# Kernel optimization log

Hardware: AMD Instinct MI355X
Metric: run time of the kernel (lower is better)

## Reference

```python
import jax, jax.numpy as jnp
import numpy as np

D_MODEL = 512
N_HEAD = 8
D_HEAD = 64
N_LAYER = 4
D_INNER = 2048
IN_CH = 2048
N_CLS = 64
B, T = 2, 2048
LN_EPS = 1e-5


def layer_norm(x, s, b):
    mu = jnp.mean(x, axis=-1, keepdims=True)
    var = jnp.mean(jnp.square(x - mu), axis=-1, keepdims=True)
    return (x - mu) * jax.lax.rsqrt(var + LN_EPS) * s + b


def rel_shift(x):
    # x: [q, k, b, n] -> Transformer-XL relative shift
    q, k, b, n = x.shape
    zp = jnp.zeros((q, 1, b, n), x.dtype)
    x = jnp.concatenate([zp, x], axis=1)          # [q, k+1, b, n]
    x = x.reshape(k + 1, q, b, n)[1:]             # drop first row
    return x.reshape(q, k, b, n)


def setup_inputs() -> dict:
    key = jax.random.key(0)
    ks = jax.random.split(key, 12)
    s = 0.02
    return {
        "x": jax.random.normal(ks[0], (B, IN_CH, T), jnp.float32),
        "emb_w": jax.random.normal(ks[1], (D_MODEL, IN_CH), jnp.float32) * s,
        "emb_b": jnp.zeros((D_MODEL,), jnp.float32),
        "r_w_bias": jax.random.normal(ks[2], (N_HEAD, D_HEAD), jnp.float32) * s,
        "r_r_bias": jax.random.normal(ks[3], (N_HEAD, D_HEAD), jnp.float32) * s,
        "qkv_w": jax.random.normal(ks[4], (N_LAYER, 3 * N_HEAD * D_HEAD, D_MODEL), jnp.float32) * s,
        "qkv_b": jnp.zeros((N_LAYER, 3 * N_HEAD * D_HEAD), jnp.float32),
        "r_proj_w": jax.random.normal(ks[5], (N_LAYER, N_HEAD * D_HEAD, D_MODEL), jnp.float32) * s,
        "o_w": jax.random.normal(ks[6], (N_LAYER, D_MODEL, N_HEAD * D_HEAD), jnp.float32) * s,
        "ln1_s": jnp.ones((N_LAYER, D_MODEL), jnp.float32),
        "ln1_b": jnp.zeros((N_LAYER, D_MODEL), jnp.float32),
        "ff1_w": jax.random.normal(ks[7], (N_LAYER, D_INNER, D_MODEL), jnp.float32) * s,
        "ff1_b": jnp.zeros((N_LAYER, D_INNER), jnp.float32),
        "ff2_w": jax.random.normal(ks[8], (N_LAYER, D_MODEL, D_INNER), jnp.float32) * s,
        "ff2_b": jnp.zeros((N_LAYER, D_MODEL), jnp.float32),
        "ln2_s": jnp.ones((N_LAYER, D_MODEL), jnp.float32),
        "ln2_b": jnp.zeros((N_LAYER, D_MODEL), jnp.float32),
        "cls_w": jax.random.normal(ks[9], (N_CLS, D_MODEL), jnp.float32) * s,
        "cls_b": jnp.zeros((N_CLS,), jnp.float32),
    }


def reference(x, emb_w, emb_b, r_w_bias, r_r_bias, qkv_w, qkv_b, r_proj_w, o_w,
              ln1_s, ln1_b, ff1_w, ff1_b, ff2_w, ff2_b, ln2_s, ln2_b, cls_w, cls_b):
    b, _, t = x.shape
    d = D_MODEL
    # 1x1 conv embedding, then to [T, B, d_model] layout as in _forward
    h = jnp.einsum('dc,bct->tbd', emb_w, x) + emb_b

    # sinusoidal positional embedding over pos_seq = klen-1 .. 0 (klen == qlen, mem_len=0)
    pos_seq = jnp.arange(t - 1, -1, -1, dtype=h.dtype)
    inv_freq = 1.0 / (10000.0 ** (jnp.arange(0, d, 2, dtype=h.dtype) / d))
    sinusoid = pos_seq[:, None] * inv_freq[None, :]
    pos_emb = jnp.concatenate([jnp.sin(sinusoid), jnp.cos(sinusoid)], axis=-1)  # [T, d]

    scale = 1.0 / (D_HEAD ** 0.5)
    for i in range(N_LAYER):
        w = h
        heads = jnp.einsum('ed,tbd->tbe', qkv_w[i], w) + qkv_b[i]          # [T,B,3*H*Dh]
        q, k, v = jnp.split(heads, 3, axis=-1)
        q = q.reshape(t, b, N_HEAD, D_HEAD)
        k = k.reshape(t, b, N_HEAD, D_HEAD)
        v = v.reshape(t, b, N_HEAD, D_HEAD)
        r_head_k = jnp.einsum('ed,td->te', r_proj_w[i], pos_emb).reshape(t, N_HEAD, D_HEAD)

        AC = jnp.einsum('ibnd,jbnd->ijbn', q + r_w_bias, k)                # content term
        BD = rel_shift(jnp.einsum('ibnd,jnd->ijbn', q + r_r_bias, r_head_k))  # position term
        attn_prob = jax.nn.softmax((AC + BD) * scale, axis=1)              # softmax over keys
        attn_vec = jnp.einsum('ijbn,jbnd->ibnd', attn_prob, v).reshape(t, b, N_HEAD * D_HEAD)
        attn_out = jnp.einsum('de,tbe->tbd', o_w[i], attn_vec)             # o_net (no bias)
        h = layer_norm(w + attn_out, ln1_s[i], ln1_b[i])                   # post-lnorm

        ff = jnp.einsum('fd,tbd->tbf', ff1_w[i], h) + ff1_b[i]
        ff = jax.nn.relu(ff)
        ff = jnp.einsum('df,tbf->tbd', ff2_w[i], ff) + ff2_b[i]
        h = layer_norm(h + ff, ln2_s[i], ln2_b[i])

    # 1x1 conv classifier -> [B, num_classes, T]
    out = jnp.einsum('kd,tbd->bkt', cls_w, h) + cls_b[None, :, None]
    return out
```

## Files before the change

kernel.cpp:

```cpp
#include <hip/hip_runtime.h>
#include <hip/hip_bf16.h>
#include <math.h>


#define T_   2048
#define B_   2
#define DM   512
#define NH   8
#define DH   64
#define DI   2048
#define INCH 2048
#define NCLS 64
#define MT   4096

typedef __attribute__((ext_vector_type(8))) short short8;
typedef __attribute__((ext_vector_type(4))) float float4v;

#define QSCALE 0.1803368801111204f

__device__ inline ushort f2bf(float f) {
  uint u = __float_as_uint(f);
  return (ushort)((u + 0x7FFFu + ((u >> 16) & 1u)) >> 16);
}
__device__ inline float bf2f(ushort h) { return __uint_as_float(((uint)h) << 16); }
__device__ inline uint pkbf(float a, float b) {
  __hip_bfloat162 h = __float22bfloat162_rn(float2{a, b});
  return *(uint*)&h;
}
__device__ inline void gload16(const void* g, void* lds) {
  __builtin_amdgcn_global_load_lds(
      (const __attribute__((address_space(1))) void*)g,
      (__attribute__((address_space(3))) void*)lds, 16, 0, 0);
}

__global__ __launch_bounds__(256) void pos_kernel(ushort* __restrict__ pe) {
  int idx = blockIdx.x * 256 + threadIdx.x;
  if (idx >= T_ * DM) return;
  int t = idx >> 9;
  int i = idx & 511;
  int j = (i < 256) ? i : (i - 256);
  double invf = exp(-(double)(2 * j) * (9.210340371976184 / 512.0));
  double a = (double)(T_ - 1 - t) * invf;
  pe[idx] = f2bf((i < 256) ? (float)sin(a) : (float)cos(a));
}

__global__ __launch_bounds__(256) void cvt6_kernel(
    const float* s0, ushort* d0, int n0,
    const float* s1, ushort* d1, int n1,
    const float* s2, ushort* d2, int n2,
    const float* s3, ushort* d3, int n3,
    const float* s4, ushort* d4, int n4,
    const float* s5, ushort* d5, int n5)
{
  const float* s; ushort* d; int n;
  switch (blockIdx.y) {
    case 0: s = s0; d = d0; n = n0; break;
    case 1: s = s1; d = d1; n = n1; break;
    case 2: s = s2; d = d2; n = n2; break;
    case 3: s = s3; d = d3; n = n3; break;
    case 4: s = s4; d = d4; n = n4; break;
    default: s = s5; d = d5; n = n5; break;
  }
  int i = blockIdx.x * 256 + threadIdx.x;
  if (i >= n) return;
  float4 v = ((const float4*)s)[i];
  ushort4 w = { f2bf(v.x), f2bf(v.y), f2bf(v.z), f2bf(v.w) };
  ((ushort4*)d)[i] = w;
}

__global__ __launch_bounds__(256) void xpose_kernel(const float* __restrict__ x,
                                                    ushort* __restrict__ xb) {
  __shared__ float s[32][33];
  int t0 = blockIdx.x * 32, k0 = blockIdx.y * 32, b = blockIdx.z;
  int tx = threadIdx.x & 31, ty = threadIdx.x >> 5;
#pragma unroll
  for (int l = 0; l < 4; ++l) {
    int k = k0 + ty + l * 8;
    s[ty + l * 8][tx] = x[((size_t)b * INCH + k) * T_ + t0 + tx];
  }
  __syncthreads();
#pragma unroll
  for (int l = 0; l < 4; ++l) {
    int t = t0 + ty + l * 8;
    xb[((size_t)(t * 2 + b)) * INCH + k0 + tx] = f2bf(s[tx][ty + l * 8]);
  }
}

__global__ __launch_bounds__(256) void vtrans_kernel(const ushort* __restrict__ heads,
                                                     ushort* __restrict__ vtg) {
  __shared__ ushort s[64][72];
  const int tid = threadIdx.x;
  int t0 = blockIdx.x * 64;
  int b = blockIdx.y & 1, n = blockIdx.y >> 1;
  for (int e = tid; e < 512; e += 256) {
    int r = e >> 3, c = e & 7;
    *(uint4*)&s[r][c * 8] =
        *(const uint4*)&heads[(size_t)((t0 + r) * 2 + b) * 1536 + 1024 + n * 64 + c * 8];
  }
  __syncthreads();
  for (int e = tid; e < 512; e += 256) {
    int d = e >> 3, c = e & 7;
    ushort tmp[8];
#pragma unroll
    for (int j = 0; j < 8; ++j) tmp[j] = s[c * 8 + j][d];
    *(uint4*)&vtg[((size_t)((b * 8 + n) * 64 + d)) * (size_t)T_ + t0 + c * 8] = *(uint4*)tmp;
  }
}

template<int TM, int OUTMODE, bool RELU>
__global__ __launch_bounds__(256) void gemm_bf16(
    const ushort* __restrict__ A, const ushort* __restrict__ W,
    const float* __restrict__ bias, float* __restrict__ Cf, ushort* __restrict__ Cb,
    int M, int N, int K)
{
  __shared__ __attribute__((aligned(16))) ushort As[TM * 64];
  __shared__ __attribute__((aligned(16))) ushort Bs[128 * 64];
  const int NI = TM / 32;
  const int tid  = threadIdx.x;
  const int wave = tid >> 6, lane = tid & 63;
  const int quad = lane >> 4, lidx = lane & 15;
  const int m0 = blockIdx.y * TM, n0 = blockIdx.x * 128;
  const int r8 = lane >> 3;
  const int cs = ((lane & 7) ^ (r8 & 7)) * 8;

  float4v acc[NI * 4];
#pragma unroll
  for (int i = 0; i < NI * 4; ++i) acc[i] = (float4v){0.f, 0.f, 0.f, 0.f};

  const int wm = (wave >> 1) * (TM / 2), wn = (wave & 1) * 64;

  for (int k0 = 0; k0 < K; k0 += 64) {
    __syncthreads();
#pragma unroll
    for (int g = 0; g < TM / 32; ++g) {
      int r0 = wave * 8 + g * 32;
      gload16(A + (size_t)(m0 + r0 + r8) * K + k0 + cs, &As[r0 * 64]);
    }
#pragma unroll
    for (int g = 0; g < 4; ++g) {
      int r0 = wave * 8 + g * 32;
      gload16(W + (size_t)(n0 + r0 + r8) * K + k0 + cs, &Bs[r0 * 64]);
    }
    __syncthreads();

#pragma unroll
    for (int kb = 0; kb < 2; ++kb) {
      short8 af[NI], bf4[4];
      const int ch = (((kb * 4 + quad) ^ (lidx & 7)) * 8);
#pragma unroll
      for (int i = 0; i < NI; ++i)
        af[i] = *(const short8*)&As[(wm + i * 16 + lidx) * 64 + ch];
#pragma unroll
      for (int j = 0; j < 4; ++j)
        bf4[j] = *(const short8*)&Bs[(wn + j * 16 + lidx) * 64 + ch];
#pragma unroll
      for (int i = 0; i < NI; ++i)
#pragma unroll
        for (int j = 0; j < 4; ++j)
          acc[i * 4 + j] = __builtin_amdgcn_mfma_f32_16x16x32_bf16(af[i], bf4[j], acc[i * 4 + j], 0, 0, 0);
    }
  }

  float bj[4];
#pragma unroll
  for (int j = 0; j < 4; ++j) bj[j] = bias ? bias[n0 + wn + j * 16 + lidx] : 0.f;
#pragma unroll
  for (int i = 0; i < NI; ++i) {
    int rbase = m0 + wm + i * 16 + quad * 4;
#pragma unroll
    for (int j = 0; j < 4; ++j) {
      int col = n0 + wn + j * 16 + lidx;
#pragma unroll
      for (int reg = 0; reg < 4; ++reg) {
        float v = acc[i * 4 + j][reg] + bj[j];
        if (RELU) v = fmaxf(v, 0.f);
        size_t off = (size_t)(rbase + reg) * N + col;
        if (OUTMODE != 1) Cf[off] = v;
        if (OUTMODE != 0) Cb[off] = f2bf(v);
      }
    }
  }
}

#define BM 128
#define BN 128
#define BK 16
#define LDT 132

__global__ __launch_bounds__(256) void gemm_f32(
    const float* __restrict__ A, const float* __restrict__ W,
    const float* __restrict__ bias, float* __restrict__ C,
    int M, int N, int K)
{
  __shared__ float Asm[BK][LDT];
  __shared__ float Wsm[BK][LDT];
  const int tid = threadIdx.x;
  const int m0 = blockIdx.y * BM;
  const int n0 = blockIdx.x * BN;
  const int row = tid >> 1;
  const int kh  = (tid & 1) * 8;
  const int ty  = tid >> 4;
  const int tx  = tid & 15;

  float acc[8][8];
#pragma unroll
  for (int i = 0; i < 8; ++i)
#pragma unroll
    for (int j = 0; j < 8; ++j) acc[i][j] = 0.f;

  for (int kt = 0; kt < K; kt += BK) {
    float a_reg[8], w_reg[8];
    {
      const float* ap = A + (size_t)(m0 + row) * K + (kt + kh);
      float4 v0 = *(const float4*)ap;
      float4 v1 = *(const float4*)(ap + 4);
      a_reg[0] = v0.x; a_reg[1] = v0.y; a_reg[2] = v0.z; a_reg[3] = v0.w;
      a_reg[4] = v1.x; a_reg[5] = v1.y; a_reg[6] = v1.z; a_reg[7] = v1.w;
    }
    {
      int nn = n0 + row;
      if (nn < N) {
        const float* wp = W + (size_t)nn * K + (kt + kh);
        float4 v0 = *(const float4*)wp;
        float4 v1 = *(const float4*)(wp + 4);
        w_reg[0] = v0.x; w_reg[1] = v0.y; w_reg[2] = v0.z; w_reg[3] = v0.w;
        w_reg[4] = v1.x; w_reg[5] = v1.y; w_reg[6] = v1.z; w_reg[7] = v1.w;
      } else {
#pragma unroll
        for (int q = 0; q < 8; ++q) w_reg[q] = 0.f;
      }
    }
    __syncthreads();
#pragma unroll
    for (int q = 0; q < 8; ++q) { Asm[kh + q][row] = a_reg[q]; Wsm[kh + q][row] = w_reg[q]; }
    __syncthreads();
#pragma unroll
    for (int k = 0; k < BK; ++k) {
      float4 a0 = *(const float4*)&Asm[k][ty * 4];
      float4 a1 = *(const float4*)&Asm[k][ty * 4 + 64];
      float4 b0 = *(const float4*)&Wsm[k][tx * 4];
      float4 b1 = *(const float4*)&Wsm[k][tx * 4 + 64];
      float av[8] = {a0.x, a0.y, a0.z, a0.w, a1.x, a1.y, a1.z, a1.w};
      float bv[8] = {b0.x, b0.y, b0.z, b0.w, b1.x, b1.y, b1.z, b1.w};
#pragma unroll
      for (int i = 0; i < 8; ++i)
#pragma unroll
        for (int j = 0; j < 8; ++j) acc[i][j] += av[i] * bv[j];
    }
  }

#pragma unroll
  for (int ih = 0; ih < 2; ++ih)
#pragma unroll
    for (int i = 0; i < 4; ++i) {
      int m = m0 + ty * 4 + ih * 64 + i;
#pragma unroll
      for (int jh = 0; jh < 2; ++jh) {
        int nn = n0 + tx * 4 + jh * 64;
        if (nn < N) {
          float4 v;
          v.x = acc[ih * 4 + i][jh * 4 + 0] + bias[nn + 0];
          v.y = acc[ih * 4 + i][jh * 4 + 1] + bias[nn + 1];
          v.z = acc[ih * 4 + i][jh * 4 + 2] + bias[nn + 2];
          v.w = acc[ih * 4 + i][jh * 4 + 3] + bias[nn + 3];
          *(float4*)&C[(size_t)m * N + nn] = v;
        }
      }
    }
}

#define GT 68

__device__ inline short8 bfrag(const char* base, int lidx, int quad, int kb) {
  return *(const short8*)(base + lidx * 128 + ((((kb << 2) + quad) ^ (lidx & 7)) << 4));
}

__global__ __launch_bounds__(256, 2) void attn_mfma_kernel(
    const ushort* __restrict__ heads, const ushort* __restrict__ rk,
    const ushort* __restrict__ vtg,
    const float* __restrict__ rwb, const float* __restrict__ rrb,
    ushort* __restrict__ avec)
{
  __shared__ __attribute__((aligned(16))) ushort Ks[64 * 64];
  __shared__ __attribute__((aligned(16))) ushort Vt[64 * 64];
  __shared__ __attribute__((aligned(16))) ushort Re[128 * 64];
  __shared__ __attribute__((aligned(16))) ushort Gbt[128 * GT];
  __shared__ __attribute__((aligned(16))) ushort Pb[64 * 64];

  const int tid  = threadIdx.x;
  const int i0   = blockIdx.x * 64;
  const int b    = blockIdx.y & 1;
  const int n    = blockIdx.y >> 1;
  const int wave = tid >> 6;
  const int lane = tid & 63;
  const int quad = lane >> 4;
  const int lidx = lane & 15;
  const int r8   = lane >> 3;
  const int cs8  = ((lane & 7) ^ (r8 & 7)) * 8;
  const int bn64 = (b * 8 + n) * 64;

  short8 qw[4][2], qr[4][2], q4[2];
  {
    auto qfrag = [&](int row, int kb, const float* bias) -> short8 {
      short8 q;
      if (row < T_) q = *(const short8*)&heads[(size_t)(row * 2 + b) * 1536 + n * 64 + kb * 32 + quad * 8];
      else { for (int t = 0; t < 8; ++t) ((ushort*)&q)[t] = 0; }
      short8 o;
#pragma unroll
      for (int t = 0; t < 8; ++t) {
        float f = (bf2f((ushort)((ushort*)&q)[t]) + bias[n * 64 + kb * 32 + quad * 8 + t]) * QSCALE;
        ((ushort*)&o)[t] = f2bf(f);
      }
      return o;
    };
#pragma unroll
    for (int rt = 0; rt < 4; ++rt) {
      int row = i0 + rt * 16 + lidx;
      qw[rt][0] = qfrag(row, 0, rwb); qw[rt][1] = qfrag(row, 1, rwb);
      qr[rt][0] = qfrag(row, 0, rrb); qr[rt][1] = qfrag(row, 1, rrb);
    }
    int row4 = i0 + 64 + lidx;
    q4[0] = qfrag(row4, 0, rrb); q4[1] = qfrag(row4, 1, rrb);
  }

  const int cfix = wave * 16 + lidx;

  int addrG0[16], addrP[16];
#pragma unroll
  for (int rt = 0; rt < 4; ++rt)
#pragma unroll
    for (int reg = 0; reg < 4; ++reg) {
      int rloc = rt * 16 + quad * 4 + reg;
      addrG0[rt * 4 + reg] = (cfix + 63 - rloc) * GT + rloc;
      addrP[rt * 4 + reg]  = rloc * 64 + (((cfix >> 3) ^ (rloc & 7)) * 8) + (cfix & 7);
    }

  float4v oacc[4], liacc[4];
#pragma unroll
  for (int rt = 0; rt < 4; ++rt) {
    oacc[rt]  = (float4v){0.f, 0.f, 0.f, 0.f};
    liacc[rt] = (float4v){0.f, 0.f, 0.f, 0.f};
  }
  short8 ones8;
#pragma unroll
  for (int t = 0; t < 8; ++t) ((ushort*)&ones8)[t] = 0x3F80;

  auto stageKRe = [&](int jt) {
    int j0 = jt * 64, qmin = j0 + 1984 - i0;
#pragma unroll
    for (int half = 0; half < 2; ++half) {
      int r0 = 8 * wave + 32 * half;
      gload16(heads + (size_t)((j0 + r0 + r8) * 2 + b) * 1536 + 512 + n * 64 + cs8, &Ks[r0 * 64]);
    }
#pragma unroll
    for (int q4i = 0; q4i < 4; ++q4i) {
      int r0 = 8 * wave + 32 * q4i;
      int qh = qmin + r0 + r8;
      int p  = (qh > T_) ? (qh - T_ - 1) : ((qh == T_) ? 0 : qh);
      gload16(rk + (size_t)p * 2048 + n * 64 + cs8, &Re[r0 * 64]);
    }
  };
  auto stageV = [&](int jt) {
    int j0 = jt * 64;
#pragma unroll
    for (int half = 0; half < 2; ++half) {
      int r0 = 8 * wave + 32 * half;
      gload16(vtg + (size_t)(bn64 + r0 + r8) * (size_t)T_ + j0 + cs8, &Vt[r0 * 64]);
    }
  };
  auto fixup = [&](int jt) {
    int qmin = jt * 64 + 1984 - i0;
    int Tidx = T_ - qmin;
    if (Tidx >= 0 && Tidx < 128) {
      if (tid < 32) ((uint*)Re)[Tidx * 32 + tid] = 0u;
      __syncthreads();
    }
  };

  stageKRe(0);
  stageV(0);
  __syncthreads();
  fixup(0);

  for (int jt = 0; jt < 32; ++jt) {
    const int qmin = jt * 64 + 1984 - i0;
    const int wth  = T_ - qmin;

    float4v sv[4];
    {
      const char* KsW = (const char*)Ks + wave * 2048;
      short8 k0 = bfrag(KsW, lidx, quad, 0);
      short8 k1 = bfrag(KsW, lidx, quad, 1);
#pragma unroll
      for (int rt = 0; rt < 4; ++rt) {
        float4v c = {0.f, 0.f, 0.f, 0.f};
        c = __builtin_amdgcn_mfma_f32_16x16x32_bf16(qw[rt][0], k0, c, 0, 0, 0);
        c = __builtin_amdgcn_mfma_f32_16x16x32_bf16(qw[rt][1], k1, c, 0, 0, 0);
        sv[rt] = c;
      }
    }
#pragma unroll
    for (int si = 0; si < 2; ++si) {
      const int ws = wave + si * 4;
      const int w0 = ws * 16;
      const char* ReW = (const char*)Re + w0 * 128;
      short8 rb0 = bfrag(ReW, lidx, quad, 0);
      short8 rb1 = bfrag(ReW, lidx, quad, 1);
#pragma unroll
      for (int rt = 0; rt < 4; ++rt) {
        bool need = si == 0 ? (rt >= 3 - wave) : (rt <= 3 - wave);
        if (need) {
          float4v g = {0.f, 0.f, 0.f, 0.f};
          g = __builtin_amdgcn_mfma_f32_16x16x32_bf16(qr[rt][0], rb0, g, 0, 0, 0);
          g = __builtin_amdgcn_mfma_f32_16x16x32_bf16(qr[rt][1], rb1, g, 0, 0, 0);
          uint2 st; st.x = pkbf(g[0], g[1]); st.y = pkbf(g[2], g[3]);
          *(uint2*)&Gbt[(w0 + lidx) * GT + rt * 16 + quad * 4] = st;
        }
      }
      if (si == 0 && wth < 63) {
        float4v g = {0.f, 0.f, 0.f, 0.f};
        g = __builtin_amdgcn_mfma_f32_16x16x32_bf16(q4[0], rb0, g, 0, 0, 0);
        g = __builtin_amdgcn_mfma_f32_16x16x32_bf16(q4[1], rb1, g, 0, 0, 0);
        if (quad == 0) Gbt[(w0 + lidx) * GT + 64] = f2bf(g[0]);
      }
    }
    __syncthreads();

    {
      const int selb = cfix + 63 - wth;
#pragma unroll
      for (int rt = 0; rt < 4; ++rt)
#pragma unroll
        for (int reg = 0; reg < 4; ++reg) {
          const int idx = rt * 4 + reg;
          const int rloc = rt * 16 + quad * 4 + reg;
          int ga = addrG0[idx] + ((rloc < selb) ? 1 : 0);
          float x = sv[rt][reg] + bf2f(Gbt[ga]);
          Pb[addrP[idx]] = f2bf(exp2f(x));
        }
    }
    __syncthreads();

    if (jt < 31) stageKRe(jt + 1);

    {
      const char* VtW = (const char*)Vt + wave * 2048;
      short8 vb0 = bfrag(VtW, lidx, quad, 0);
      short8 vb1 = bfrag(VtW, lidx, quad, 1);
#pragma unroll
      for (int rt = 0; rt < 4; ++rt) {
        const char* PbW = (const char*)Pb + rt * 2048;
        short8 pa0 = bfrag(PbW, lidx, quad, 0);
        short8 pa1 = bfrag(PbW, lidx, quad, 1);
        oacc[rt]  = __builtin_amdgcn_mfma_f32_16x16x32_bf16(pa0, vb0, oacc[rt], 0, 0, 0);
        oacc[rt]  = __builtin_amdgcn_mfma_f32_16x16x32_bf16(pa1, vb1, oacc[rt], 0, 0, 0);
        liacc[rt] = __builtin_amdgcn_mfma_f32_16x16x32_bf16(pa0, ones8, liacc[rt], 0, 0, 0);
        liacc[rt] = __builtin_amdgcn_mfma_f32_16x16x32_bf16(pa1, ones8, liacc[rt], 0, 0, 0);
      }
    }
    __syncthreads();

    if (jt < 31) {
      stageV(jt + 1);
      fixup(jt + 1);
    }
  }

#pragma unroll
  for (int rt = 0; rt < 4; ++rt)
#pragma unroll
    for (int reg = 0; reg < 4; ++reg) {
      int i = i0 + rt * 16 + quad * 4 + reg;
      float val = oacc[rt][reg] / liacc[rt][reg];
      avec[(size_t)(i * 2 + b) * DM + n * 64 + wave * 16 + lidx] = f2bf(val);
    }
}

__global__ __launch_bounds__(256) void ln_res_kernel(
    float* __restrict__ h, ushort* __restrict__ hb, const float* __restrict__ delta,
    const float* __restrict__ s, const float* __restrict__ bb)
{
  const int m = blockIdx.x;
  const int tid = threadIdx.x;
  float* hp = h + (size_t)m * DM;
  ushort* hbp = hb + (size_t)m * DM;
  const float* dp = delta + (size_t)m * DM;
  float x0 = hp[tid] + dp[tid];
  float x1 = hp[tid + 256] + dp[tid + 256];
  float sum = x0 + x1, sq = x0 * x0 + x1 * x1;
#pragma unroll
  for (int o = 32; o > 0; o >>= 1) { sum += __shfl_down(sum, o); sq += __shfl_down(sq, o); }
  __shared__ float part[8];
  int wv = tid >> 6;
  if ((tid & 63) == 0) { part[wv * 2] = sum; part[wv * 2 + 1] = sq; }
  __syncthreads();
  float ts = part[0] + part[2] + part[4] + part[6];
  float tq = part[1] + part[3] + part[5] + part[7];
  float mu = ts * (1.f / DM);
  float var = tq * (1.f / DM) - mu * mu;
  float rs = rsqrtf(var + 1e-5f);
  float y0 = (x0 - mu) * rs * s[tid]       + bb[tid];
  float y1 = (x1 - mu) * rs * s[tid + 256] + bb[tid + 256];
  hp[tid] = y0;       hbp[tid] = f2bf(y0);
  hp[tid + 256] = y1; hbp[tid + 256] = f2bf(y1);
}

__global__ __launch_bounds__(256) void reorder_kernel(const float* __restrict__ ct,
                                                      float* __restrict__ out) {
  int idx = blockIdx.x * 256 + threadIdx.x;
  if (idx >= B_ * NCLS * T_) return;
  int t  = idx & (T_ - 1);
  int nc = (idx >> 11) & 63;
  int bb = idx >> 17;
  out[idx] = ct[(size_t)(t * B_ + bb) * NCLS + nc];
}

extern "C" void kernel_launch(void* const* d_in, const int* in_sizes, int n_in,
                              void* d_out, int out_size, void* d_ws, size_t ws_size,
                              hipStream_t stream)
{
  const float* x     = (const float*)d_in[0];
  const float* emb_w = (const float*)d_in[1];
  const float* emb_b = (const float*)d_in[2];
  const float* rwb   = (const float*)d_in[3];
  const float* rrb   = (const float*)d_in[4];
  const float* qkv_w = (const float*)d_in[5];
  const float* qkv_b = (const float*)d_in[6];
  const float* rproj = (const float*)d_in[7];
  const float* o_w   = (const float*)d_in[8];
  const float* ln1s  = (const float*)d_in[9];
  const float* ln1b  = (const float*)d_in[10];
  const float* ff1w  = (const float*)d_in[11];
  const float* ff1b  = (const float*)d_in[12];
  const float* ff2w  = (const float*)d_in[13];
  const float* ff2b  = (const float*)d_in[14];
  const float* ln2s  = (const float*)d_in[15];
  const float* ln2b  = (const float*)d_in[16];
  const float* clsw  = (const float*)d_in[17];
  const float* clsb  = (const float*)d_in[18];
  float* out = (float*)d_out;

  char* p = (char*)d_ws;
  float*  h       = (float*)p;   p += (size_t)MT * DM * 4;
  float*  tmpf    = (float*)p;   p += (size_t)MT * DM * 4;
  ushort* hb      = (ushort*)p;  p += (size_t)MT * DM * 2;
  ushort* headsb  = (ushort*)p;  p += (size_t)MT * 1536 * 2;
  ushort* peb     = (ushort*)p;  p += (size_t)T_ * DM * 2;
  ushort* rk_all  = (ushort*)p;  p += (size_t)T_ * 2048 * 2;
  ushort* avecb   = (ushort*)p;  p += (size_t)MT * DM * 2;
  ushort* xfb     = (ushort*)p;  p += (size_t)MT * INCH * 2;
  ushort* emb_wb  = (ushort*)p;  p += (size_t)DM * INCH * 2;
  ushort* qkv_wb  = (ushort*)p;  p += (size_t)4 * 1536 * DM * 2;
  ushort* rproj_wb= (ushort*)p;  p += (size_t)4 * DM * DM * 2;
  ushort* o_wb    = (ushort*)p;  p += (size_t)4 * DM * DM * 2;
  ushort* ff1_wb  = (ushort*)p;  p += (size_t)4 * DI * DM * 2;
  ushort* ff2_wb  = (ushort*)p;  p += (size_t)4 * DM * DI * 2;
  ushort* vtg     = xfb;

  cvt6_kernel<<<dim3(4096, 6), 256, 0, stream>>>(
      emb_w, emb_wb, DM * INCH / 4,
      qkv_w, qkv_wb, 4 * 1536 * DM / 4,
      rproj, rproj_wb, 4 * DM * DM / 4,
      o_w,   o_wb,   4 * DM * DM / 4,
      ff1w,  ff1_wb, 4 * DI * DM / 4,
      ff2w,  ff2_wb, 4 * DM * DI / 4);
  pos_kernel<<<(T_ * DM) / 256, 256, 0, stream>>>(peb);
  xpose_kernel<<<dim3(T_ / 32, INCH / 32, B_), 256, 0, stream>>>(x, xfb);

  gemm_bf16<64, 2, false><<<dim3(DM / 128, MT / 64), 256, 0, stream>>>(
      xfb, emb_wb, emb_b, h, hb, MT, DM, INCH);
  gemm_bf16<128, 1, false><<<dim3(2048 / 128, T_ / 128), 256, 0, stream>>>(
      peb, rproj_wb, nullptr, nullptr, rk_all, T_, 2048, DM);

  for (int l = 0; l < 4; ++l) {
    gemm_bf16<128, 1, false><<<dim3(1536 / 128, MT / 128), 256, 0, stream>>>(
        hb, qkv_wb + (size_t)l * 1536 * DM, qkv_b + l * 1536, nullptr, headsb, MT, 1536, DM);
    vtrans_kernel<<<dim3(T_ / 64, B_ * NH), 256, 0, stream>>>(headsb, vtg);
    attn_mfma_kernel<<<dim3(T_ / 64, B_ * NH), 256, 0, stream>>>(
        headsb, rk_all + (size_t)l * 512, vtg, rwb, rrb, avecb);
    gemm_bf16<32, 0, false><<<dim3(DM / 128, MT / 32), 256, 0, stream>>>(
        avecb, o_wb + (size_t)l * DM * DM, nullptr, tmpf, nullptr, MT, DM, DM);
    ln_res_kernel<<<MT, 256, 0, stream>>>(h, hb, tmpf, ln1s + l * DM, ln1b + l * DM);
    gemm_bf16<128, 1, true><<<dim3(DI / 128, MT / 128), 256, 0, stream>>>(
        hb, ff1_wb + (size_t)l * DI * DM, ff1b + l * DI, nullptr, xfb, MT, DI, DM);
    gemm_bf16<32, 0, false><<<dim3(DM / 128, MT / 32), 256, 0, stream>>>(
        xfb, ff2_wb + (size_t)l * DM * DI, ff2b + l * DM, tmpf, nullptr, MT, DM, DI);
    ln_res_kernel<<<MT, 256, 0, stream>>>(h, hb, tmpf, ln2s + l * DM, ln2b + l * DM);
  }

  gemm_f32<<<dim3(1, MT / BM), 256, 0, stream>>>(h, clsw, clsb, tmpf, MT, NCLS, DM);
  reorder_kernel<<<(B_ * NCLS * T_) / 256, 256, 0, stream>>>(tmpf, out);
}
```

Baseline: 974.1 us.

## Keep attention probabilities in registers via transposed score tiles and permlane swaps

Each wave now owns 16 query rows instead of 16 key columns. The score MFMA is computed in transposed form so that the softmax probabilities can be packed to bf16 with v_cvt_pk_bf16_f32 and rearranged into A-operand fragments with permlane32/16 swaps. This removes the Pb shared-memory round trip and one __syncthreads per key tile. It also cuts the row-sum MFMAs from eight to two per tile and issues the next K/Re staging earlier. The cost is more register pressure and reliance on gfx950 permlane swap instructions, whose lane mapping has to be exactly right.

```diff
diff --git a/kernel.cpp b/kernel.cpp
--- a/kernel.cpp
+++ b/kernel.cpp
@@ -285,7 +285,6 @@
   __shared__ __attribute__((aligned(16))) ushort Vt[64 * 64];
   __shared__ __attribute__((aligned(16))) ushort Re[128 * 64];
   __shared__ __attribute__((aligned(16))) ushort Gbt[128 * GT];
-  __shared__ __attribute__((aligned(16))) ushort Pb[64 * 64];
 
   const int tid  = threadIdx.x;
   const int i0   = blockIdx.x * 64;
@@ -298,8 +297,9 @@
   const int r8   = lane >> 3;
   const int cs8  = ((lane & 7) ^ (r8 & 7)) * 8;
   const int bn64 = (b * 8 + n) * 64;
-
-  short8 qw[4][2], qr[4][2], q4[2];
+  const int rloc = wave * 16 + lidx;
+
+  short8 qw[2], qr4[4][2], q4[2];
   {
     auto qfrag = [&](int row, int kb, const float* bias) -> short8 {
       short8 q;
@@ -313,34 +313,26 @@
       }
       return o;
     };
+    qw[0] = qfrag(i0 + rloc, 0, rwb);
+    qw[1] = qfrag(i0 + rloc, 1, rwb);
 #pragma unroll
     for (int rt = 0; rt < 4; ++rt) {
       int row = i0 + rt * 16 + lidx;
-      qw[rt][0] = qfrag(row, 0, rwb); qw[rt][1] = qfrag(row, 1, rwb);
-      qr[rt][0] = qfrag(row, 0, rrb); qr[rt][1] = qfrag(row, 1, rrb);
+      qr4[rt][0] = qfrag(row, 0, rrb); qr4[rt][1] = qfrag(row, 1, rrb);
     }
     int row4 = i0 + 64 + lidx;
     q4[0] = qfrag(row4, 0, rrb); q4[1] = qfrag(row4, 1, rrb);
   }
 
-  const int cfix = wave * 16 + lidx;
-
-  int addrG0[16], addrP[16];
-#pragma unroll
-  for (int rt = 0; rt < 4; ++rt)
-#pragma unroll
-    for (int reg = 0; reg < 4; ++reg) {
-      int rloc = rt * 16 + quad * 4 + reg;
-      addrG0[rt * 4 + reg] = (cfix + 63 - rloc) * GT + rloc;
-      addrP[rt * 4 + reg]  = rloc * 64 + (((cfix >> 3) ^ (rloc & 7)) * 8) + (cfix & 7);
-    }
-
-  float4v oacc[4], liacc[4];
-#pragma unroll
-  for (int rt = 0; rt < 4; ++rt) {
-    oacc[rt]  = (float4v){0.f, 0.f, 0.f, 0.f};
-    liacc[rt] = (float4v){0.f, 0.f, 0.f, 0.f};
-  }
+  int a0[4];
+#pragma unroll
+  for (int t = 0; t < 4; ++t)
+    a0[t] = (t * 16 + quad * 4 + 63 - rloc) * GT + rloc;
+
+  float4v oacc[4];
+  float4v liacc = (float4v){0.f, 0.f, 0.f, 0.f};
+#pragma unroll
+  for (int dt = 0; dt < 4; ++dt) oacc[dt] = (float4v){0.f, 0.f, 0.f, 0.f};
   short8 ones8;
 #pragma unroll
   for (int t = 0; t < 8; ++t) ((ushort*)&ones8)[t] = 0x3F80;
@@ -387,18 +379,17 @@
     const int wth  = T_ - qmin;
 
     float4v sv[4];
-    {
-      const char* KsW = (const char*)Ks + wave * 2048;
-      short8 k0 = bfrag(KsW, lidx, quad, 0);
-      short8 k1 = bfrag(KsW, lidx, quad, 1);
-#pragma unroll
-      for (int rt = 0; rt < 4; ++rt) {
-        float4v c = {0.f, 0.f, 0.f, 0.f};
-        c = __builtin_amdgcn_mfma_f32_16x16x32_bf16(qw[rt][0], k0, c, 0, 0, 0);
-        c = __builtin_amdgcn_mfma_f32_16x16x32_bf16(qw[rt][1], k1, c, 0, 0, 0);
-        sv[rt] = c;
-      }
-    }
+#pragma unroll
+    for (int t = 0; t < 4; ++t) {
+      const char* KsT = (const char*)Ks + t * 2048;
+      short8 kf0 = bfrag(KsT, lidx, quad, 0);
+      short8 kf1 = bfrag(KsT, lidx, quad, 1);
+      float4v c = {0.f, 0.f, 0.f, 0.f};
+      c = __builtin_amdgcn_mfma_f32_16x16x32_bf16(kf0, qw[0], c, 0, 0, 0);
+      c = __builtin_amdgcn_mfma_f32_16x16x32_bf16(kf1, qw[1], c, 0, 0, 0);
+      sv[t] = c;
+    }
+
 #pragma unroll
     for (int si = 0; si < 2; ++si) {
       const int ws = wave + si * 4;
@@ -411,8 +402,8 @@
         bool need = si == 0 ? (rt >= 3 - wave) : (rt <= 3 - wave);
         if (need) {
           float4v g = {0.f, 0.f, 0.f, 0.f};
-          g = __builtin_amdgcn_mfma_f32_16x16x32_bf16(qr[rt][0], rb0, g, 0, 0, 0);
-          g = __builtin_amdgcn_mfma_f32_16x16x32_bf16(qr[rt][1], rb1, g, 0, 0, 0);
+          g = __builtin_amdgcn_mfma_f32_16x16x32_bf16(qr4[rt][0], rb0, g, 0, 0, 0);
+          g = __builtin_amdgcn_mfma_f32_16x16x32_bf16(qr4[rt][1], rb1, g, 0, 0, 0);
           uint2 st; st.x = pkbf(g[0], g[1]); st.y = pkbf(g[2], g[3]);
           *(uint2*)&Gbt[(w0 + lidx) * GT + rt * 16 + quad * 4] = st;
         }
@@ -426,54 +417,73 @@
     }
     __syncthreads();
 
+    if (jt < 31) stageKRe(jt + 1);
+
     {
-      const int selb = cfix + 63 - wth;
-#pragma unroll
-      for (int rt = 0; rt < 4; ++rt)
-#pragma unroll
-        for (int reg = 0; reg < 4; ++reg) {
-          const int idx = rt * 4 + reg;
-          const int rloc = rt * 16 + quad * 4 + reg;
-          int ga = addrG0[idx] + ((rloc < selb) ? 1 : 0);
-          float x = sv[rt][reg] + bf2f(Gbt[ga]);
-          Pb[addrP[idx]] = f2bf(exp2f(x));
+      const int cth = wth + rloc - 63;
+#pragma unroll
+      for (int t = 0; t < 4; ++t) {
+        const int c0 = t * 16 + quad * 4;
+#pragma unroll
+        for (int r = 0; r < 4; ++r) {
+          int ga = a0[t] + r * GT + ((c0 + r > cth) ? 1 : 0);
+          sv[t][r] = exp2f(sv[t][r] + bf2f(Gbt[ga]));
         }
-    }
-    __syncthreads();
-
-    if (jt < 31) stageKRe(jt + 1);
-
-    {
-      const char* VtW = (const char*)Vt + wave * 2048;
-      short8 vb0 = bfrag(VtW, lidx, quad, 0);
-      short8 vb1 = bfrag(VtW, lidx, quad, 1);
-#pragma unroll
-      for (int rt = 0; rt < 4; ++rt) {
-        const char* PbW = (const char*)Pb + rt * 2048;
-        short8 pa0 = bfrag(PbW, lidx, quad, 0);
-        short8 pa1 = bfrag(PbW, lidx, quad, 1);
-        oacc[rt]  = __builtin_amdgcn_mfma_f32_16x16x32_bf16(pa0, vb0, oacc[rt], 0, 0, 0);
-        oacc[rt]  = __builtin_amdgcn_mfma_f32_16x16x32_bf16(pa1, vb1, oacc[rt], 0, 0, 0);
-        liacc[rt] = __builtin_amdgcn_mfma_f32_16x16x32_bf16(pa0, ones8, liacc[rt], 0, 0, 0);
-        liacc[rt] = __builtin_amdgcn_mfma_f32_16x16x32_bf16(pa1, ones8, liacc[rt], 0, 0, 0);
-      }
-    }
+      }
+    }
+
+    short8 vb[4][2];
+#pragma unroll
+    for (int dt = 0; dt < 4; ++dt) {
+      const char* VtT = (const char*)Vt + dt * 2048;
+      vb[dt][0] = bfrag(VtT, lidx, quad, 0);
+      vb[dt][1] = bfrag(VtT, lidx, quad, 1);
+    }
+
+    short8 af[2];
+#pragma unroll
+    for (int kb = 0; kb < 2; ++kb) {
+      uint mm[4];
+#pragma unroll
+      for (int i = 0; i < 2; ++i) {
+        uint e, o;
+        asm("v_cvt_pk_bf16_f32 %0, %1, %2" : "=v"(e) : "v"(sv[2 * kb][2 * i]),     "v"(sv[2 * kb][2 * i + 1]));
+        asm("v_cvt_pk_bf16_f32 %0, %1, %2" : "=v"(o) : "v"(sv[2 * kb + 1][2 * i]), "v"(sv[2 * kb + 1][2 * i + 1]));
+        asm("v_permlane32_swap_b32 %0, %1" : "+v"(e), "+v"(o));
+        asm("v_permlane16_swap_b32 %0, %1" : "+v"(e), "+v"(o));
+        mm[i] = e; mm[2 + i] = o;
+      }
+      union { uint u[4]; short8 s; } cv;
+      cv.u[0] = mm[0]; cv.u[1] = mm[1]; cv.u[2] = mm[2]; cv.u[3] = mm[3];
+      af[kb] = cv.s;
+    }
+
     __syncthreads();
 
     if (jt < 31) {
       stageV(jt + 1);
       fixup(jt + 1);
     }
-  }
-
-#pragma unroll
-  for (int rt = 0; rt < 4; ++rt)
-#pragma unroll
-    for (int reg = 0; reg < 4; ++reg) {
-      int i = i0 + rt * 16 + quad * 4 + reg;
-      float val = oacc[rt][reg] / liacc[rt][reg];
-      avec[(size_t)(i * 2 + b) * DM + n * 64 + wave * 16 + lidx] = f2bf(val);
-    }
+
+#pragma unroll
+    for (int dt = 0; dt < 4; ++dt) {
+      oacc[dt] = __builtin_amdgcn_mfma_f32_16x16x32_bf16(af[0], vb[dt][0], oacc[dt], 0, 0, 0);
+      oacc[dt] = __builtin_amdgcn_mfma_f32_16x16x32_bf16(af[1], vb[dt][1], oacc[dt], 0, 0, 0);
+    }
+    liacc = __builtin_amdgcn_mfma_f32_16x16x32_bf16(af[0], ones8, liacc, 0, 0, 0);
+    liacc = __builtin_amdgcn_mfma_f32_16x16x32_bf16(af[1], ones8, liacc, 0, 0, 0);
+  }
+
+#pragma unroll
+  for (int reg = 0; reg < 4; ++reg) {
+    int i = i0 + wave * 16 + quad * 4 + reg;
+    float li = liacc[reg];
+#pragma unroll
+    for (int dt = 0; dt < 4; ++dt) {
+      float val = oacc[dt][reg] / li;
+      avec[(size_t)(i * 2 + b) * DM + n * 64 + dt * 16 + lidx] = f2bf(val);
+    }
+  }
 }
 
 __global__ __launch_bounds__(256) void ln_res_kernel(
```

New measurement: 925.3 us. 1.05x faster.
